# Kernel optimization log

Measured on AMD Instinct MI355X. Metric: run time of the kernel, lower is better.

## Reference

```python
import jax, jax.numpy as jnp
import numpy as np

DIM = 512; HW = 8; B = 64; L = 2 * HW * HW  # 128, fixed by mlp_b Linear(128,1)
D_STATE = 16; D_CONV = 4; D_INNER = 2 * DIM; DT_RANK = 32  # ceil(512/16)


def setup_inputs() -> dict:
    key = jax.random.key(0)
    ks = jax.random.split(key, 12)
    f = lambda i, shape, s=0.02: jax.random.normal(ks[i], shape, dtype=jnp.float32) * s
    return {
        "spt_fts": jax.random.normal(ks[0], (B, DIM, HW, HW), dtype=jnp.float32),
        "qry_fts": jax.random.normal(ks[1], (B, DIM, HW, HW), dtype=jnp.float32),
        "conv_w": f(2, (DIM, DIM, 3)),
        "conv_b": jnp.zeros((DIM,), jnp.float32),
        "ln_w": jnp.ones((DIM,), jnp.float32),
        "ln_b": jnp.zeros((DIM,), jnp.float32),
        "in_proj_w": f(3, (2 * D_INNER, DIM)),
        "conv1d_w": f(4, (D_INNER, 1, D_CONV)),
        "conv1d_b": jnp.zeros((D_INNER,), jnp.float32),
        "x_proj_w": f(5, (DT_RANK + 2 * D_STATE, D_INNER)),
        "dt_proj_w": f(6, (D_INNER, DT_RANK)),
        "dt_proj_b": f(7, (D_INNER,), 0.5),
        "A_log": jnp.log(jnp.broadcast_to(jnp.arange(1, D_STATE + 1, dtype=jnp.float32), (D_INNER, D_STATE))),
        "D_skip": jnp.ones((D_INNER,), jnp.float32),
        "out_proj_w": f(8, (DIM, D_INNER)),
        "mlp_a_w": f(9, (1, DIM)),
        "mlp_a_b": jnp.zeros((1,), jnp.float32),
        "mlp_b_w": f(10, (1, L)),
        "mlp_b_b": jnp.zeros((1,), jnp.float32),
    }


def _ln(x, w, b, eps=1e-5):
    mu = x.mean(-1, keepdims=True)
    var = ((x - mu) ** 2).mean(-1, keepdims=True)
    return (x - mu) * jax.lax.rsqrt(var + eps) * w + b


def _mamba(u, in_proj_w, conv1d_w, conv1d_b, x_proj_w, dt_proj_w, dt_proj_b, A_log, D_skip, out_proj_w):
    # u: (B, L, DIM)
    Bb = u.shape[0]
    xz = u @ in_proj_w.T                       # (B, L, 2*D_INNER)
    x, z = jnp.split(xz, 2, axis=-1)
    # causal depthwise conv (pad d_conv-1 left, truncate to L as in mamba_ssm)
    xc = jax.lax.conv_general_dilated(
        x.transpose(0, 2, 1), conv1d_w, (1,), [(D_CONV - 1, 0)],
        dimension_numbers=("NCH", "OIH", "NCH"), feature_group_count=D_INNER,
    ) + conv1d_b[None, :, None]
    x = jax.nn.silu(xc).transpose(0, 2, 1)     # (B, L, D_INNER)
    dbc = x @ x_proj_w.T                       # (B, L, DT_RANK + 2*D_STATE)
    dt = jax.nn.softplus(dbc[..., :DT_RANK] @ dt_proj_w.T + dt_proj_b)  # (B, L, D_INNER)
    Bm = dbc[..., DT_RANK:DT_RANK + D_STATE]   # (B, L, D_STATE)
    Cm = dbc[..., DT_RANK + D_STATE:]          # (B, L, D_STATE)
    A = -jnp.exp(A_log)                        # (D_INNER, D_STATE)

    def step(h, ins):
        dt_t, x_t, B_t, C_t = ins              # (B,Di), (B,Di), (B,N), (B,N)
        h = jnp.exp(dt_t[..., None] * A) * h + (dt_t * x_t)[..., None] * B_t[:, None, :]
        return h, jnp.einsum("bdn,bn->bd", h, C_t)

    h0 = jnp.zeros((Bb, D_INNER, D_STATE), u.dtype)
    _, ys = jax.lax.scan(step, h0, (dt.transpose(1, 0, 2), x.transpose(1, 0, 2), Bm.transpose(1, 0, 2), Cm.transpose(1, 0, 2)))
    y = ys.transpose(1, 0, 2) + x * D_skip
    return (y * jax.nn.silu(z)) @ out_proj_w.T  # (B, L, DIM)


def reference(spt_fts, qry_fts, conv_w, conv_b, ln_w, ln_b, in_proj_w, conv1d_w, conv1d_b,
              x_proj_w, dt_proj_w, dt_proj_b, A_log, D_skip, out_proj_w,
              mlp_a_w, mlp_a_b, mlp_b_w, mlp_b_b):
    Bb, dim, h, w = spt_fts.shape
    s = spt_fts.reshape(Bb, h * w, dim)        # torch .view = raw reshape
    q = qry_fts.reshape(Bb, h * w, dim)
    fts = jnp.concatenate([s, q], axis=1).transpose(0, 2, 1)  # (B, dim, L)
    fts = jax.lax.conv_general_dilated(fts, conv_w, (1,), "SAME",
                                       dimension_numbers=("NCH", "OIH", "NCH")) + conv_b[None, :, None]
    fts = _ln(fts.transpose(0, 2, 1), ln_w, ln_b).transpose(0, 2, 1)
    fts = jax.nn.relu(fts)
    m = _mamba(fts.transpose(0, 2, 1), in_proj_w, conv1d_w, conv1d_b, x_proj_w,
               dt_proj_w, dt_proj_b, A_log, D_skip, out_proj_w).transpose(0, 2, 1)
    fts = m + fts
    fts = _ln(fts.transpose(0, 2, 1), ln_w, ln_b).transpose(0, 2, 1)
    coff = (fts.transpose(0, 2, 1) @ mlp_a_w.T + mlp_a_b)[..., 0]  # (B, L)
    coff = coff @ mlp_b_w[0] + mlp_b_b[0]                          # (B,)
    return jax.nn.sigmoid(coff)
```

## Files before the change

### kernel.cpp

```cpp
#include <hip/hip_runtime.h>
#include <cstdint>
#include <cstddef>

typedef unsigned short u16;
typedef __attribute__((ext_vector_type(8))) short short8;
typedef __attribute__((ext_vector_type(4))) float floatx4;

__device__ __forceinline__ float b2f(u16 u) {
  union { uint32_t i; float f; } v; v.i = ((uint32_t)u) << 16; return v.f;
}
__device__ __forceinline__ u16 f2b(float f) {
  union { float f; uint32_t i; } v; v.f = f;
  uint32_t x = v.i;
  return (u16)((x + 0x7fffu + ((x >> 16) & 1u)) >> 16);
}
__device__ __forceinline__ float rdw(const void* p, size_t i, int flag) {
  return flag ? ((const float*)p)[i] : b2f(((const u16*)p)[i]);
}
__device__ __forceinline__ void gll16(const u16* g, u16* l) {
  __builtin_amdgcn_global_load_lds(
      (const __attribute__((address_space(1))) void*)g,
      (__attribute__((address_space(3))) void*)l, 16, 0, 0);
}

struct P19 { const void* p[19]; };
struct Sz19 { int n[19]; };

__global__ __launch_bounds__(256) void k_detect(P19 ps, Sz19 sz, int* flags) {
  __shared__ int sdeg[4], snz[4];
  const int ti = blockIdx.x;
  const int n = sz.n[ti];
  const u16* p = (const u16*)ps.p[ti];
  int m = n / 2; if (m > 256) m = 256;
  int deg = 0, nz = 0;
  const int j = threadIdx.x;
  if (j < m) {
    u16 e = p[2 * j], o = p[2 * j + 1];
    float a = fabsf(b2f(e));
    deg = (e == 0 || !(a <= 1e6f) || a < 1e-8f) ? 1 : 0;
    nz = (e != 0 || o != 0) ? 1 : 0;
  }
#pragma unroll
  for (int off = 32; off; off >>= 1) {
    deg += __shfl_down(deg, off, 64);
    nz  += __shfl_down(nz, off, 64);
  }
  if ((j & 63) == 0) { sdeg[j >> 6] = deg; snz[j >> 6] = nz; }
  __syncthreads();
  if (j == 0) {
    int d = sdeg[0] + sdeg[1] + sdeg[2] + sdeg[3];
    int z = snz[0] + snz[1] + snz[2] + snz[3];
    flags[ti] = (n >= 4 && z > 0 && d * 10 >= m * 7) ? 1 : 0;
  }
}

__global__ void k_sentinel(float* out, float val) {
  int i = threadIdx.x;
  if (i < 64) out[i] = val;
}

__global__ __launch_bounds__(256) void k_cvt2(const void* s0, const void* s1,
                                              const int* flags, u16* __restrict__ dst) {
  unsigned e = blockIdx.x * 2048u + threadIdx.x * 8u;
  if (e >= 4194304u) return;
  const int si = (e >= 2097152u) ? 1 : 0;
  const void* src = si ? s1 : s0;
  unsigned local = e & 2097151u;
  if (flags[si]) {
    const float* f = (const float*)src + local;
    float4 v0 = *(const float4*)f;
    float4 v1 = *(const float4*)(f + 4);
    u16 o[8] = {f2b(v0.x), f2b(v0.y), f2b(v0.z), f2b(v0.w),
                f2b(v1.x), f2b(v1.y), f2b(v1.z), f2b(v1.w)};
    *(uint4*)(dst + e) = *(const uint4*)o;
  } else {
    *(uint4*)(dst + e) = *(const uint4*)((const u16*)src + local);
  }
}

__global__ __launch_bounds__(256) void k_small(P19 ps, int* flags,
    u16* __restrict__ tb, float* __restrict__ af, u16* __restrict__ zbuf) {
  const int blk = blockIdx.x, t = threadIdx.x;
  if (blk < 64) {
    int i = blk * 256 + t;
    af[i] = -__expf(rdw(ps.p[12], i, flags[12]));
    return;
  }
  if (blk < 101) {
    int i = (blk - 64) * 256 + t;
    if (i >= 9346) return;
    const int cum[12] = {0,512,1024,1536,5632,6656,7680,8704,9216,9217,9345,9346};
    const int sidx[11] = {3,4,5,7,8,11,13,15,16,17,18};
    int s = 10;
#pragma unroll
    for (int k = 10; k > 0; --k) if (i < cum[k]) s = k - 1;
    int si = sidx[s];
    tb[i] = f2b(rdw(ps.p[si], i - cum[s], flags[si]));
    return;
  }
  if (t < 32) zbuf[t] = 0;
  if (t == 0) {
    int okf = 1;
    for (int n = 0; n < 16; ++n) {
      float ref = logf((float)(n + 1));
      float v0 = rdw(ps.p[12], n, flags[12]);
      float v1 = rdw(ps.p[12], 500 * 16 + n, flags[12]);
      if (fabsf(v0 - ref) > 1e-3f || fabsf(v1 - ref) > 1e-3f) okf = 0;
    }
    flags[20] = okf;
  }
}

__global__ __launch_bounds__(256) void k_wfrag2(
    const void* __restrict__ src, int Nact, int Ksrc, int nkt,
    u16* __restrict__ dst, int totalChunks, const int* flags, int fidx, int isconv)
{
  int c = blockIdx.x * 256 + threadIdx.x;
  if (c >= totalChunks) return;
  const int flag = flags[fidx];
  const int blk = c >> 9, w = c & 511;
  const int nt = blk / nkt, kt = blk - nt * nkt;
  const int grp = w >> 6, lane = w & 63;
  const int kq = lane >> 4, fm = lane & 15;
  const int n = nt * 128 + grp * 16 + fm;
  const int k0 = kt * 32 + kq * 8;
  u16 o[8];
#pragma unroll
  for (int j = 0; j < 8; ++j) {
    const int k = k0 + j;
    float v = 0.f;
    if (n < Nact && k < Ksrc) {
      size_t si = isconv ? ((size_t)(n * 512 + (k & 511)) * 3 + (k >> 9))
                         : ((size_t)n * Ksrc + k);
      v = rdw(src, si, flag);
    }
    o[j] = f2b(v);
  }
  *(uint4*)(dst + (size_t)c * 8) = *(const uint4*)o;
}

template <int ACT, int CONV>
__global__ __launch_bounds__(256) void k_mgemm2(
    const u16* __restrict__ A, int lda,
    const u16* __restrict__ A2, const u16* __restrict__ zbuf,
    const u16* __restrict__ Bpk, int nkt,
    u16* __restrict__ C, int ldc, int K, int Nact,
    const u16* __restrict__ bias,
    const u16* __restrict__ addsrc, int ldadd, int b0)
{
  __shared__ __align__(16) u16 Asw[128 * 128];
  const int t = threadIdx.x;
  int nt = blockIdx.x, mt = blockIdx.y;
  if ((gridDim.y & 7) == 0) {
    const int lin = mt * gridDim.x + nt;
    const int xcd = lin & 7, slot = lin >> 3;
    const int MT8 = gridDim.y >> 3;
    mt = xcd * MT8 + (slot % MT8);
    nt = slot / MT8;
  }
  const int n0 = nt * 128, m0 = mt * 128;
  const int wave = t >> 6, lane = t & 63;
  const int wr = wave >> 1, wc = wave & 1;
  const int fm = lane & 15, kq = lane >> 4;
  const int srow = lane >> 4, spos = lane & 15;

  floatx4 acc[4][4];
#pragma unroll
  for (int i = 0; i < 4; ++i)
#pragma unroll
    for (int j = 0; j < 4; ++j)
      acc[i][j] = (floatx4){0.f, 0.f, 0.f, 0.f};

  const u16* bbase = Bpk + (size_t)nt * nkt * 4096 + ((size_t)(wc * 4) * 64 + lane) * 8;

  const int niter = (K + 127) >> 7;
  for (int kt = 0; kt < niter; ++kt) {
    __syncthreads();
#pragma unroll
    for (int j = 0; j < 8; ++j) {
      const int i = wave * 8 + j;
      const int row = 4 * i + srow;
      const int kq_src = spos ^ (row & 15);
      const int kabs = kt * 128 + kq_src * 8;
      const u16* src;
      if (CONV) {
        const int seg = kabs >> 9, ii = kabs & 511;
        const int lp = row + seg - 1;
        src = (lp < 0 || lp > 127) ? zbuf
            : (lp < 64 ? A  + (((size_t)(b0 + mt) * 64 + lp) << 9) + ii
                       : A2 + (((size_t)(b0 + mt) * 64 + (lp - 64)) << 9) + ii);
      } else {
        src = A + (size_t)(m0 + row) * lda + kabs;
      }
      gll16(src, Asw + (size_t)i * 512);
    }
    __syncthreads();
#pragma unroll
    for (int s = 0; s < 4; ++s) {
      short8 bfr[4];
      const u16* bp2 = bbase + (size_t)(kt * 4 + s) * 4096;
#pragma unroll
      for (int nj = 0; nj < 4; ++nj)
        bfr[nj] = *(const short8*)(bp2 + nj * 512);
      short8 afr[4];
      const int kga = s * 4 + kq;
#pragma unroll
      for (int mi = 0; mi < 4; ++mi) {
        const int row = wr * 64 + mi * 16 + fm;
        afr[mi] = *(const short8*)(Asw + row * 128 + ((kga ^ fm) * 8));
      }
#pragma unroll
      for (int mi = 0; mi < 4; ++mi)
#pragma unroll
        for (int nj = 0; nj < 4; ++nj)
          acc[mi][nj] = __builtin_amdgcn_mfma_f32_16x16x32_bf16(
              afr[mi], bfr[nj], acc[mi][nj], 0, 0, 0);
    }
  }

  const int orow = (lane >> 4) * 4;
  const int ocol = lane & 15;
#pragma unroll
  for (int nj = 0; nj < 4; ++nj) {
    const int col = n0 + wc * 64 + nj * 16 + ocol;
    if (col >= Nact) continue;
    const float bv = bias ? b2f(bias[col]) : 0.f;
#pragma unroll
    for (int mi = 0; mi < 4; ++mi) {
#pragma unroll
      for (int reg = 0; reg < 4; ++reg) {
        const int row = m0 + wr * 64 + mi * 16 + orow + reg;
        float v = acc[mi][nj][reg] + bv;
        if (addsrc) v += b2f(addsrc[(size_t)row * ldadd + col]);
        if (ACT == 1) v = (v > 20.f) ? v : log1pf(__expf(v));
        C[(size_t)row * ldc + col] = f2b(v);
      }
    }
  }
}

__global__ __launch_bounds__(256) void k_lnrelu2(
    u16* __restrict__ u, const u16* __restrict__ lnw, const u16* __restrict__ lnb)
{
  const int row = blockIdx.x * 4 + (threadIdx.x >> 6);
  const int lane = threadIdx.x & 63;
  u16* p = u + (size_t)row * 512 + lane * 8;
  uint4 v = *(const uint4*)p;
  const u16* va = (const u16*)&v;
  float x[8];
  float s = 0.f, ss = 0.f;
#pragma unroll
  for (int i = 0; i < 8; ++i) { x[i] = b2f(va[i]); s += x[i]; ss += x[i] * x[i]; }
#pragma unroll
  for (int off = 32; off; off >>= 1) {
    s += __shfl_xor(s, off, 64);
    ss += __shfl_xor(ss, off, 64);
  }
  float mean = s * (1.f / 512.f), var = ss * (1.f / 512.f) - mean * mean;
  float inv = rsqrtf(var + 1e-5f);
  uint4 wv = *(const uint4*)(lnw + lane * 8);
  uint4 bv = *(const uint4*)(lnb + lane * 8);
  const u16* wa = (const u16*)&wv; const u16* ba = (const u16*)&bv;
  u16 o[8];
#pragma unroll
  for (int i = 0; i < 8; ++i)
    o[i] = f2b(fmaxf((x[i] - mean) * inv * b2f(wa[i]) + b2f(ba[i]), 0.f));
  *(uint4*)p = *(const uint4*)o;
}

__global__ __launch_bounds__(256) void k_dwconv2(
    const u16* __restrict__ xz, const u16* __restrict__ c1wb,
    const u16* __restrict__ c1bb, u16* __restrict__ xs)
{
  const int l = blockIdx.x, b = blockIdx.y;
  const int d4 = threadIdx.x * 4;
  float w[4][4];
#pragma unroll
  for (int i = 0; i < 4; ++i) {
    uint2 wv = *(const uint2*)(c1wb + (d4 + i) * 4);
    const u16* wa = (const u16*)&wv;
    w[i][0] = b2f(wa[0]); w[i][1] = b2f(wa[1]);
    w[i][2] = b2f(wa[2]); w[i][3] = b2f(wa[3]);
  }
  uint2 bv = *(const uint2*)(c1bb + d4);
  const u16* ba = (const u16*)&bv;
  float acc[4] = {b2f(ba[0]), b2f(ba[1]), b2f(ba[2]), b2f(ba[3])};
#pragma unroll
  for (int k = 0; k < 4; ++k) {
    int ls = l + k - 3;
    if (ls >= 0) {
      uint2 xv = *(const uint2*)(xz + ((size_t)b * 128 + ls) * 2048 + d4);
      const u16* xa = (const u16*)&xv;
#pragma unroll
      for (int i = 0; i < 4; ++i) acc[i] += b2f(xa[i]) * w[i][k];
    }
  }
  u16 o[4];
#pragma unroll
  for (int i = 0; i < 4; ++i) o[i] = f2b(acc[i] / (1.f + __expf(-acc[i])));
  *(uint2*)(xs + ((size_t)b * 128 + l) * 1024 + d4) = *(const uint2*)o;
}

__global__ __launch_bounds__(256) void k_scan6(
    const u16* __restrict__ dt, const u16* __restrict__ xs,
    const u16* __restrict__ dbc, const u16* __restrict__ xz,
    const float* __restrict__ af, const u16* __restrict__ dskb,
    u16* __restrict__ g, const int* __restrict__ flags)
{
  __shared__ __align__(16) float BC[128][32];
  __shared__ __align__(16) u16 DTs[2][32 * 128];
  __shared__ __align__(16) u16 XSs[2][32 * 128];
  __shared__ __align__(16) u16 Y[64 * 128];
  const int b = blockIdx.y, t = threadIdx.x;
  const int d0 = blockIdx.x * 128;
  const int dg = t >> 1;
  const int nh = (t & 1) * 8;
  const int d = d0 + dg;
  const int fast = flags[20];

#pragma unroll
  for (int i = t; i < 4096; i += 256) {
    int l = i >> 5, c = i & 31;
    BC[l][c] = b2f(dbc[((size_t)b * 128 + l) * 64 + 32 + c]);
  }
  float av[8], h[8];
#pragma unroll
  for (int j = 0; j < 8; ++j) h[j] = 0.f;
  if (!fast) {
#pragma unroll
    for (int j = 0; j < 8; ++j) av[j] = af[(size_t)d * 16 + nh + j];
  }
  const float dsk = b2f(dskb[d]);

  const int wv = t >> 6, ln = t & 63;
  const int sd = (ln & 15) * 8;
  const size_t gb = (size_t)b * 128 * 1024 + d0 + sd;

#pragma unroll
  for (int p = 0; p < 2; ++p) {
    const int row = p * 16 + wv * 4 + (ln >> 4);
    const size_t src = gb + (size_t)row * 1024;
    gll16(dt + src, &DTs[0][(p * 16 + wv * 4) * 128]);
    gll16(xs + src, &XSs[0][(p * 16 + wv * 4) * 128]);
  }
  __syncthreads();

  for (int c = 0; c < 4; ++c) {
    const int buf = c & 1;
    if (c < 3) {
#pragma unroll
      for (int p = 0; p < 2; ++p) {
        const int row = p * 16 + wv * 4 + (ln >> 4);
        const size_t src = gb + (size_t)((c + 1) * 32 + row) * 1024;
        gll16(dt + src, &DTs[buf ^ 1][(p * 16 + wv * 4) * 128]);
        gll16(xs + src, &XSs[buf ^ 1][(p * 16 + wv * 4) * 128]);
      }
    }
#pragma unroll 4
    for (int li = 0; li < 32; ++li) {
      const float dtv = b2f(DTs[buf][li * 128 + dg]);
      const float xv  = b2f(XSs[buf][li * 128 + dg]);
      const float dx = dtv * xv;
      float m[8];
      if (fast) {
        const float q = __expf(-dtv);
        const float q2 = q * q, q4 = q2 * q2, q8 = q4 * q4;
        const float base = nh ? q8 : 1.f;
        m[0] = base * q;
#pragma unroll
        for (int j = 1; j < 8; ++j) m[j] = m[j - 1] * q;
      } else {
#pragma unroll
        for (int j = 0; j < 8; ++j) m[j] = __expf(dtv * av[j]);
      }
      const int l = c * 32 + li;
      float4 B0 = *(const float4*)&BC[l][nh];
      float4 B1 = *(const float4*)&BC[l][nh + 4];
      float4 C0 = *(const float4*)&BC[l][16 + nh];
      float4 C1 = *(const float4*)&BC[l][16 + nh + 4];
      float y;
      h[0] = m[0] * h[0] + dx * B0.x; y = h[0] * C0.x;
      h[1] = m[1] * h[1] + dx * B0.y; y = fmaf(h[1], C0.y, y);
      h[2] = m[2] * h[2] + dx * B0.z; y = fmaf(h[2], C0.z, y);
      h[3] = m[3] * h[3] + dx * B0.w; y = fmaf(h[3], C0.w, y);
      h[4] = m[4] * h[4] + dx * B1.x; y = fmaf(h[4], C1.x, y);
      h[5] = m[5] * h[5] + dx * B1.y; y = fmaf(h[5], C1.y, y);
      h[6] = m[6] * h[6] + dx * B1.z; y = fmaf(h[6], C1.z, y);
      h[7] = m[7] * h[7] + dx * B1.w; y = fmaf(h[7], C1.w, y);
      y += __shfl_xor(y, 1, 64);
      if (nh == 0) Y[(l & 63) * 128 + dg] = f2b(y + xv * dsk);
    }
    __syncthreads();
    if (c & 1) {
      const int lb = (c >> 1) * 64;
#pragma unroll
      for (int i = t; i < 2048; i += 256) {
        const int lr = i >> 4, dn = (i & 15) * 8;
        const int l = lb + lr;
        uint4 yv = *(const uint4*)&Y[lr * 128 + dn];
        uint4 zv = *(const uint4*)(xz + ((size_t)b * 128 + l) * 2048 + 1024 + d0 + dn);
        const u16* ya = (const u16*)&yv; const u16* za = (const u16*)&zv;
        u16 o[8];
#pragma unroll
        for (int j = 0; j < 8; ++j) {
          float z = b2f(za[j]);
          o[j] = f2b(b2f(ya[j]) * (z / (1.f + __expf(-z))));
        }
        *(uint4*)(g + ((size_t)b * 128 + l) * 1024 + d0 + dn) = *(const uint4*)o;
      }
      __syncthreads();
    }
  }
}

__global__ __launch_bounds__(256) void k_ln2b(
    const u16* __restrict__ fts, const u16* __restrict__ lnw,
    const u16* __restrict__ lnb, const u16* __restrict__ maw,
    const u16* __restrict__ mab, float* __restrict__ coff)
{
  const int row = blockIdx.x * 4 + (threadIdx.x >> 6);
  const int lane = threadIdx.x & 63;
  const u16* p = fts + (size_t)row * 512 + lane * 8;
  uint4 v = *(const uint4*)p;
  const u16* va = (const u16*)&v;
  float x[8];
  float s = 0.f, ss = 0.f;
#pragma unroll
  for (int i = 0; i < 8; ++i) { x[i] = b2f(va[i]); s += x[i]; ss += x[i] * x[i]; }
#pragma unroll
  for (int off = 32; off; off >>= 1) {
    s += __shfl_xor(s, off, 64);
    ss += __shfl_xor(ss, off, 64);
  }
  float mean = s * (1.f / 512.f), var = ss * (1.f / 512.f) - mean * mean;
  float inv = rsqrtf(var + 1e-5f);
  uint4 wv = *(const uint4*)(lnw + lane * 8);
  uint4 bv = *(const uint4*)(lnb + lane * 8);
  uint4 mv = *(const uint4*)(maw + lane * 8);
  const u16* wa = (const u16*)&wv; const u16* ba = (const u16*)&bv;
  const u16* ma = (const u16*)&mv;
  float dot = 0.f;
#pragma unroll
  for (int i = 0; i < 8; ++i)
    dot += ((x[i] - mean) * inv * b2f(wa[i]) + b2f(ba[i])) * b2f(ma[i]);
#pragma unroll
  for (int off = 32; off; off >>= 1) dot += __shfl_xor(dot, off, 64);
  if (lane == 0) coff[row] = dot + b2f(mab[0]);
}

__global__ void k_final(const float* __restrict__ coff, const u16* __restrict__ mbw,
                        const u16* __restrict__ mbb, float* __restrict__ out, int b0)
{
  __shared__ float red[2];
  const int b = blockIdx.x, t = threadIdx.x;
  float v = coff[(size_t)b * 128 + t] * b2f(mbw[t]);
#pragma unroll
  for (int off = 32; off; off >>= 1) v += __shfl_xor(v, off, 64);
  if ((t & 63) == 0) red[t >> 6] = v;
  __syncthreads();
  if (t == 0) {
    float x = red[0] + red[1] + b2f(mbb[0]);
    out[b0 + b] = 1.f / (1.f + __expf(-x));
  }
}

extern "C" void kernel_launch(void* const* d_in, const int* in_sizes, int n_in,
                              void* d_out, int out_size, void* d_ws, size_t ws_size,
                              hipStream_t stream)
{
  (void)out_size;
  static const int expect[19] = {
    2097152, 2097152, 786432, 512, 512, 512, 1048576, 4096, 1024, 65536,
    32768, 1024, 16384, 1024, 524288, 512, 1, 128, 1 };
  bool ok = (n_in == 19);
  if (ok) for (int i = 0; i < 19; ++i) if (in_sizes[i] != expect[i]) { ok = false; break; }
  if (!ok) { k_sentinel<<<1, 64, 0, stream>>>((float*)d_out, 2.0f); return; }

  const size_t ACT0 = 6857960, PER_B = 794880;
  int Bc = 64;
  while (Bc > 1 && 2 * (ACT0 + (size_t)Bc * PER_B) > ws_size) Bc >>= 1;
  if (2 * (ACT0 + PER_B) > ws_size) {
    k_sentinel<<<1, 64, 0, stream>>>((float*)d_out, 3.0f);
    return;
  }

  int* flags = (int*)d_ws;
  u16* zbuf  = (u16*)d_ws + 64;
  u16* sptb  = (u16*)d_ws + 96;
  u16* qryb  = sptb  + 2097152;
  u16* ipwPk = qryb  + 2097152;
  u16* W2Pk  = ipwPk + 1048576;
  u16* xpwPk = W2Pk  + 786432;
  u16* dpwPk = xpwPk + 131072;
  u16* opwPk = dpwPk + 131072;
  u16* TB    = opwPk + 524288;
  u16* cbb   = TB;
  u16* lnwb  = TB + 512;
  u16* lnbb  = TB + 1024;
  u16* c1wb  = TB + 1536;
  u16* c1bb  = TB + 5632;
  u16* dpbb  = TB + 6656;
  u16* dskb  = TB + 7680;
  u16* mawb  = TB + 8704;
  u16* mabb  = TB + 9216;
  u16* mbwb  = TB + 9217;
  u16* mbbb  = TB + 9345;
  float* af  = (float*)((u16*)d_ws + 6825192);
  u16* ACT   = (u16*)d_ws + ACT0;
  u16* u_  = ACT;
  u16* xz  = u_  + (size_t)Bc * 65536;
  u16* xs  = xz  + (size_t)Bc * 262144;
  u16* dt  = xs  + (size_t)Bc * 131072;
  u16* dbc = dt  + (size_t)Bc * 131072;
  u16* g   = dbc + (size_t)Bc * 8192;
  u16* fts = g   + (size_t)Bc * 131072;
  float* coff = (float*)(fts + (size_t)Bc * 65536);

  P19 ps; Sz19 sz;
  for (int i = 0; i < 19; ++i) { ps.p[i] = d_in[i]; sz.n[i] = in_sizes[i]; }
  k_detect<<<19, 256, 0, stream>>>(ps, sz, flags);
  k_cvt2<<<2048, 256, 0, stream>>>(d_in[0], d_in[1], flags, sptb);
  k_small<<<102, 256, 0, stream>>>(ps, flags, TB, af, zbuf);
  k_wfrag2<<<512, 256, 0, stream>>>(d_in[6],  2048,  512, 16, ipwPk, 131072, flags, 6, 0);
  k_wfrag2<<<384, 256, 0, stream>>>(d_in[2],   512, 1536, 48, W2Pk,   98304, flags, 2, 1);
  k_wfrag2<<< 64, 256, 0, stream>>>(d_in[9],    64, 1024, 32, xpwPk,  16384, flags, 9, 0);
  k_wfrag2<<< 64, 256, 0, stream>>>(d_in[10], 1024,   32,  4, dpwPk,  16384, flags, 10, 0);
  k_wfrag2<<<256, 256, 0, stream>>>(d_in[14],  512, 1024, 32, opwPk,  65536, flags, 14, 0);

  for (int b0 = 0; b0 < 64; b0 += Bc) {
    k_mgemm2<0, 1><<<dim3(4, Bc), 256, 0, stream>>>(sptb, 0, qryb, zbuf,
        W2Pk, 48, u_, 512, 1536, 512, cbb, nullptr, 0, b0);
    k_lnrelu2<<<dim3(Bc * 32), 256, 0, stream>>>(u_, lnwb, lnbb);
    k_mgemm2<0, 0><<<dim3(16, Bc), 256, 0, stream>>>(u_, 512, nullptr, zbuf,
        ipwPk, 16, xz, 2048, 512, 2048, nullptr, nullptr, 0, 0);
    k_dwconv2<<<dim3(128, Bc), 256, 0, stream>>>(xz, c1wb, c1bb, xs);
    k_mgemm2<0, 0><<<dim3(1, Bc), 256, 0, stream>>>(xs, 1024, nullptr, zbuf,
        xpwPk, 32, dbc, 64, 1024, 64, nullptr, nullptr, 0, 0);
    k_mgemm2<1, 0><<<dim3(8, Bc), 256, 0, stream>>>(dbc, 64, nullptr, zbuf,
        dpwPk, 4, dt, 1024, 128, 1024, dpbb, nullptr, 0, 0);
    k_scan6<<<dim3(8, Bc), 256, 0, stream>>>(dt, xs, dbc, xz, af, dskb, g, flags);
    k_mgemm2<0, 0><<<dim3(4, Bc), 256, 0, stream>>>(g, 1024, nullptr, zbuf,
        opwPk, 32, fts, 512, 1024, 512, nullptr, u_, 512, 0);
    k_ln2b<<<dim3(Bc * 32), 256, 0, stream>>>(fts, lnwb, lnbb, mawb, mabb, coff);
    k_final<<<dim3(Bc), 128, 0, stream>>>(coff, mbwb, mbbb, (float*)d_out, b0);
  }
}
```

Before: 406.4 us.

## Fuse depthwise conv into in_proj GEMM epilogue and dt_proj into scan

The in_proj GEMM now applies the causal depthwise conv and SiLU in its epilogue for the x half of the output tiles. It stages the 128-row accumulator tile in swizzled LDS and writes xs directly, which removes the separate dwconv kernel and its re-read of xz. The scan kernel now computes dt_proj plus softplus in-block with MFMA from the dbc tile, so the dt tensor is no longer written to and read back from global memory. This cuts two launches and intermediate traffic, but adds LDS usage and extra work to the GEMM and scan blocks, and relies on a full 128-length sequence fitting in one M tile.

```diff
diff --git a/kernel.cpp b/kernel.cpp
--- a/kernel.cpp
+++ b/kernel.cpp
@@ -139,16 +139,20 @@
   *(uint4*)(dst + (size_t)c * 8) = *(const uint4*)o;
 }
 
-template <int ACT, int CONV>
+template <int ACT, int CONV, int DWC>
 __global__ __launch_bounds__(256) void k_mgemm2(
     const u16* __restrict__ A, int lda,
     const u16* __restrict__ A2, const u16* __restrict__ zbuf,
     const u16* __restrict__ Bpk, int nkt,
     u16* __restrict__ C, int ldc, int K, int Nact,
     const u16* __restrict__ bias,
-    const u16* __restrict__ addsrc, int ldadd, int b0)
+    const u16* __restrict__ addsrc, int ldadd, int b0,
+    const u16* __restrict__ c1wb, const u16* __restrict__ c1bb,
+    u16* __restrict__ xs_out)
 {
   __shared__ __align__(16) u16 Asw[128 * 128];
+  __shared__ __align__(16) u16 CW[512];
+  __shared__ __align__(16) u16 CB[128];
   const int t = threadIdx.x;
   int nt = blockIdx.x, mt = blockIdx.y;
   if ((gridDim.y & 7) == 0) {
@@ -220,6 +224,68 @@
 
   const int orow = (lane >> 4) * 4;
   const int ocol = lane & 15;
+
+  if (DWC && nt < 8) {
+    __syncthreads();
+    u16* T = Asw;
+#pragma unroll
+    for (int nj = 0; nj < 4; ++nj) {
+      const int col = wc * 64 + nj * 16 + ocol;
+#pragma unroll
+      for (int mi = 0; mi < 4; ++mi) {
+#pragma unroll
+        for (int reg = 0; reg < 4; ++reg) {
+          const int row = wr * 64 + mi * 16 + orow + reg;
+          T[row * 128 + (col ^ ((row & 7) << 4))] = f2b(acc[mi][nj][reg]);
+        }
+      }
+    }
+    for (int i = t; i < 640; i += 256) {
+      if (i < 512) CW[i] = c1wb[nt * 512 + i];
+      else CB[i - 512] = c1bb[nt * 128 + (i - 512)];
+    }
+    __syncthreads();
+    const int r = t >> 1, ch = (t & 1) * 64;
+#pragma unroll
+    for (int c8 = 0; c8 < 8; ++c8) {
+      const int cb_ = ch + c8 * 8;
+      float accv[8];
+      {
+        uint4 bv = *(const uint4*)&CB[cb_];
+        const u16* ba = (const u16*)&bv;
+#pragma unroll
+        for (int j = 0; j < 8; ++j) accv[j] = b2f(ba[j]);
+      }
+      float wj[8][4];
+#pragma unroll
+      for (int q = 0; q < 4; ++q) {
+        uint4 wv = *(const uint4*)&CW[(cb_ + q * 2) * 4];
+        const u16* wa = (const u16*)&wv;
+        wj[q * 2][0] = b2f(wa[0]); wj[q * 2][1] = b2f(wa[1]);
+        wj[q * 2][2] = b2f(wa[2]); wj[q * 2][3] = b2f(wa[3]);
+        wj[q * 2 + 1][0] = b2f(wa[4]); wj[q * 2 + 1][1] = b2f(wa[5]);
+        wj[q * 2 + 1][2] = b2f(wa[6]); wj[q * 2 + 1][3] = b2f(wa[7]);
+      }
+#pragma unroll
+      for (int k = 0; k < 4; ++k) {
+        const int rt = r - 3 + k;
+        if (rt >= 0) {
+          uint4 tv = *(const uint4*)&T[rt * 128 + (cb_ ^ ((rt & 7) << 4))];
+          const u16* ta = (const u16*)&tv;
+#pragma unroll
+          for (int j = 0; j < 8; ++j) accv[j] += b2f(ta[j]) * wj[j][k];
+        }
+      }
+      u16 o[8];
+#pragma unroll
+      for (int j = 0; j < 8; ++j)
+        o[j] = f2b(accv[j] / (1.f + __expf(-accv[j])));
+      *(uint4*)(xs_out + ((size_t)(mt * 128 + r) * 1024 + nt * 128 + cb_)) =
+          *(const uint4*)o;
+    }
+    return;
+  }
+
 #pragma unroll
   for (int nj = 0; nj < 4; ++nj) {
     const int col = n0 + wc * 64 + nj * 16 + ocol;
@@ -268,61 +334,87 @@
   *(uint4*)p = *(const uint4*)o;
 }
 
-__global__ __launch_bounds__(256) void k_dwconv2(
-    const u16* __restrict__ xz, const u16* __restrict__ c1wb,
-    const u16* __restrict__ c1bb, u16* __restrict__ xs)
-{
-  const int l = blockIdx.x, b = blockIdx.y;
-  const int d4 = threadIdx.x * 4;
-  float w[4][4];
-#pragma unroll
-  for (int i = 0; i < 4; ++i) {
-    uint2 wv = *(const uint2*)(c1wb + (d4 + i) * 4);
-    const u16* wa = (const u16*)&wv;
-    w[i][0] = b2f(wa[0]); w[i][1] = b2f(wa[1]);
-    w[i][2] = b2f(wa[2]); w[i][3] = b2f(wa[3]);
-  }
-  uint2 bv = *(const uint2*)(c1bb + d4);
-  const u16* ba = (const u16*)&bv;
-  float acc[4] = {b2f(ba[0]), b2f(ba[1]), b2f(ba[2]), b2f(ba[3])};
-#pragma unroll
-  for (int k = 0; k < 4; ++k) {
-    int ls = l + k - 3;
-    if (ls >= 0) {
-      uint2 xv = *(const uint2*)(xz + ((size_t)b * 128 + ls) * 2048 + d4);
-      const u16* xa = (const u16*)&xv;
-#pragma unroll
-      for (int i = 0; i < 4; ++i) acc[i] += b2f(xa[i]) * w[i][k];
-    }
-  }
-  u16 o[4];
-#pragma unroll
-  for (int i = 0; i < 4; ++i) o[i] = f2b(acc[i] / (1.f + __expf(-acc[i])));
-  *(uint2*)(xs + ((size_t)b * 128 + l) * 1024 + d4) = *(const uint2*)o;
-}
-
-__global__ __launch_bounds__(256) void k_scan6(
-    const u16* __restrict__ dt, const u16* __restrict__ xs,
-    const u16* __restrict__ dbc, const u16* __restrict__ xz,
-    const float* __restrict__ af, const u16* __restrict__ dskb,
-    u16* __restrict__ g, const int* __restrict__ flags)
+__global__ __launch_bounds__(256) void k_scan7(
+    const u16* __restrict__ xs, const u16* __restrict__ dbc,
+    const u16* __restrict__ xz, const u16* __restrict__ dpwPk,
+    const u16* __restrict__ dpbb, const float* __restrict__ af,
+    const u16* __restrict__ dskb, u16* __restrict__ g,
+    const int* __restrict__ flags)
 {
   __shared__ __align__(16) float BC[128][32];
-  __shared__ __align__(16) u16 DTs[2][32 * 128];
+  __shared__ __align__(16) u16 DT[128 * 128];
   __shared__ __align__(16) u16 XSs[2][32 * 128];
-  __shared__ __align__(16) u16 Y[64 * 128];
+  __shared__ __align__(16) u16 YD[64 * 128];
   const int b = blockIdx.y, t = threadIdx.x;
-  const int d0 = blockIdx.x * 128;
-  const int dg = t >> 1;
-  const int nh = (t & 1) * 8;
+  const int nt = blockIdx.x;
+  const int d0 = nt * 128;
+  const int dg = t >> 1, nh = (t & 1) * 8;
   const int d = d0 + dg;
   const int fast = flags[20];
-
-#pragma unroll
+  const int wave = t >> 6, lane = t & 63;
+  const int wr = wave >> 1, wc = wave & 1;
+  const int fm = lane & 15, kg = lane >> 4;
+
+  u16* DBC = YD;
+  for (int i = t; i < 1024; i += 256) {
+    const int row = i >> 3, chn = (i & 7) * 8;
+    *(uint4*)&DBC[row * 64 + chn] =
+        *(const uint4*)(dbc + ((size_t)b * 128 + row) * 64 + chn);
+  }
   for (int i = t; i < 4096; i += 256) {
-    int l = i >> 5, c = i & 31;
+    const int l = i >> 5, c = i & 31;
     BC[l][c] = b2f(dbc[((size_t)b * 128 + l) * 64 + 32 + c]);
   }
+  const int sd = (lane & 15) * 8;
+  const size_t gb = (size_t)b * 128 * 1024 + d0 + sd;
+#pragma unroll
+  for (int p = 0; p < 2; ++p) {
+    const int row = p * 16 + wave * 4 + (lane >> 4);
+    gll16(xs + gb + (size_t)row * 1024, &XSs[0][(p * 16 + wave * 4) * 128]);
+  }
+  __syncthreads();
+
+  {
+    floatx4 dacc[4][4];
+#pragma unroll
+    for (int i = 0; i < 4; ++i)
+#pragma unroll
+      for (int j = 0; j < 4; ++j)
+        dacc[i][j] = (floatx4){0.f, 0.f, 0.f, 0.f};
+    short8 bfr[4], afr[4];
+#pragma unroll
+    for (int nj = 0; nj < 4; ++nj)
+      bfr[nj] = *(const short8*)(dpwPk +
+          ((size_t)(nt * 4) * 512 + (size_t)(wc * 4 + nj) * 64 + lane) * 8);
+#pragma unroll
+    for (int mi = 0; mi < 4; ++mi)
+      afr[mi] = *(const short8*)&DBC[(wr * 64 + mi * 16 + fm) * 64 + kg * 8];
+#pragma unroll
+    for (int mi = 0; mi < 4; ++mi)
+#pragma unroll
+      for (int nj = 0; nj < 4; ++nj)
+        dacc[mi][nj] = __builtin_amdgcn_mfma_f32_16x16x32_bf16(
+            afr[mi], bfr[nj], dacc[mi][nj], 0, 0, 0);
+    const int orow = (lane >> 4) * 4, ocol = lane & 15;
+#pragma unroll
+    for (int nj = 0; nj < 4; ++nj) {
+      const int col = wc * 64 + nj * 16 + ocol;
+      const float bv = b2f(dpbb[d0 + col]);
+#pragma unroll
+      for (int mi = 0; mi < 4; ++mi) {
+#pragma unroll
+        for (int reg = 0; reg < 4; ++reg) {
+          const int row = wr * 64 + mi * 16 + orow + reg;
+          float v = dacc[mi][nj][reg] + bv;
+          v = (v > 20.f) ? v : log1pf(__expf(v));
+          DT[row * 128 + col] = f2b(v);
+        }
+      }
+    }
+  }
+  __syncthreads();
+
+  u16* Y = YD;
   float av[8], h[8];
 #pragma unroll
   for (int j = 0; j < 8; ++j) h[j] = 0.f;
@@ -331,34 +423,21 @@
     for (int j = 0; j < 8; ++j) av[j] = af[(size_t)d * 16 + nh + j];
   }
   const float dsk = b2f(dskb[d]);
-
-  const int wv = t >> 6, ln = t & 63;
-  const int sd = (ln & 15) * 8;
-  const size_t gb = (size_t)b * 128 * 1024 + d0 + sd;
-
-#pragma unroll
-  for (int p = 0; p < 2; ++p) {
-    const int row = p * 16 + wv * 4 + (ln >> 4);
-    const size_t src = gb + (size_t)row * 1024;
-    gll16(dt + src, &DTs[0][(p * 16 + wv * 4) * 128]);
-    gll16(xs + src, &XSs[0][(p * 16 + wv * 4) * 128]);
-  }
-  __syncthreads();
 
   for (int c = 0; c < 4; ++c) {
     const int buf = c & 1;
     if (c < 3) {
 #pragma unroll
       for (int p = 0; p < 2; ++p) {
-        const int row = p * 16 + wv * 4 + (ln >> 4);
-        const size_t src = gb + (size_t)((c + 1) * 32 + row) * 1024;
-        gll16(dt + src, &DTs[buf ^ 1][(p * 16 + wv * 4) * 128]);
-        gll16(xs + src, &XSs[buf ^ 1][(p * 16 + wv * 4) * 128]);
+        const int row = p * 16 + wave * 4 + (lane >> 4);
+        gll16(xs + gb + (size_t)((c + 1) * 32 + row) * 1024,
+              &XSs[buf ^ 1][(p * 16 + wave * 4) * 128]);
       }
     }
 #pragma unroll 4
     for (int li = 0; li < 32; ++li) {
-      const float dtv = b2f(DTs[buf][li * 128 + dg]);
+      const int l = c * 32 + li;
+      const float dtv = b2f(DT[l * 128 + dg]);
       const float xv  = b2f(XSs[buf][li * 128 + dg]);
       const float dx = dtv * xv;
       float m[8];
@@ -373,7 +452,6 @@
 #pragma unroll
         for (int j = 0; j < 8; ++j) m[j] = __expf(dtv * av[j]);
       }
-      const int l = c * 32 + li;
       float4 B0 = *(const float4*)&BC[l][nh];
       float4 B1 = *(const float4*)&BC[l][nh + 4];
       float4 C0 = *(const float4*)&BC[l][16 + nh];
@@ -528,19 +606,17 @@
   k_wfrag2<<<256, 256, 0, stream>>>(d_in[14],  512, 1024, 32, opwPk,  65536, flags, 14, 0);
 
   for (int b0 = 0; b0 < 64; b0 += Bc) {
-    k_mgemm2<0, 1><<<dim3(4, Bc), 256, 0, stream>>>(sptb, 0, qryb, zbuf,
-        W2Pk, 48, u_, 512, 1536, 512, cbb, nullptr, 0, b0);
+    k_mgemm2<0, 1, 0><<<dim3(4, Bc), 256, 0, stream>>>(sptb, 0, qryb, zbuf,
+        W2Pk, 48, u_, 512, 1536, 512, cbb, nullptr, 0, b0, nullptr, nullptr, nullptr);
     k_lnrelu2<<<dim3(Bc * 32), 256, 0, stream>>>(u_, lnwb, lnbb);
-    k_mgemm2<0, 0><<<dim3(16, Bc), 256, 0, stream>>>(u_, 512, nullptr, zbuf,
-        ipwPk, 16, xz, 2048, 512, 2048, nullptr, nullptr, 0, 0);
-    k_dwconv2<<<dim3(128, Bc), 256, 0, stream>>>(xz, c1wb, c1bb, xs);
-    k_mgemm2<0, 0><<<dim3(1, Bc), 256, 0, stream>>>(xs, 1024, nullptr, zbuf,
-        xpwPk, 32, dbc, 64, 1024, 64, nullptr, nullptr, 0, 0);
-    k_mgemm2<1, 0><<<dim3(8, Bc), 256, 0, stream>>>(dbc, 64, nullptr, zbuf,
-        dpwPk, 4, dt, 1024, 128, 1024, dpbb, nullptr, 0, 0);
-    k_scan6<<<dim3(8, Bc), 256, 0, stream>>>(dt, xs, dbc, xz, af, dskb, g, flags);
-    k_mgemm2<0, 0><<<dim3(4, Bc), 256, 0, stream>>>(g, 1024, nullptr, zbuf,
-        opwPk, 32, fts, 512, 1024, 512, nullptr, u_, 512, 0);
+    k_mgemm2<0, 0, 1><<<dim3(16, Bc), 256, 0, stream>>>(u_, 512, nullptr, zbuf,
+        ipwPk, 16, xz, 2048, 512, 2048, nullptr, nullptr, 0, 0, c1wb, c1bb, xs);
+    k_mgemm2<0, 0, 0><<<dim3(1, Bc), 256, 0, stream>>>(xs, 1024, nullptr, zbuf,
+        xpwPk, 32, dbc, 64, 1024, 64, nullptr, nullptr, 0, 0, nullptr, nullptr, nullptr);
+    k_scan7<<<dim3(8, Bc), 256, 0, stream>>>(xs, dbc, xz, dpwPk, dpbb,
+                                             af, dskb, g, flags);
+    k_mgemm2<0, 0, 0><<<dim3(4, Bc), 256, 0, stream>>>(g, 1024, nullptr, zbuf,
+        opwPk, 32, fts, 512, 1024, 512, nullptr, u_, 512, 0, nullptr, nullptr, nullptr);
     k_ln2b<<<dim3(Bc * 32), 256, 0, stream>>>(fts, lnwb, lnbb, mawb, mabb, coff);
     k_final<<<dim3(Bc), 128, 0, stream>>>(coff, mbwb, mbbb, (float*)d_out, b0);
   }
```

After: 350.3 us. 13.8% less time.
